# Kernel tuning notes

Hardware: AMD Instinct MI355X
Metric: run time of the kernel (lower is better)

Reference implementation:

```python
import jax, jax.numpy as jnp
import numpy as np

B, R = 2, 4096
N_COARSE, N_IMP = 48, 48
RAY_START, RAY_END = 0.1, 1.0
BOX_WARP = 2.0
C_PLANE, H_PLANE = 32, 256
HIDDEN = 64

_P = np.array([[[1, 0, 0], [0, 1, 0], [0, 0, 1]],
               [[1, 0, 0], [0, 0, 1], [0, 1, 0]],
               [[0, 0, 1], [1, 0, 0], [0, 1, 0]]], np.float32)
INV_PLANES = jnp.asarray(np.linalg.inv(_P))  # [3,3,3]


def _gs_one(f, g):
    # f: [C,H,W]; g: [M,2] in [-1,1]; bilinear, zeros padding, align_corners=False
    C, H, W = f.shape
    x = (g[:, 0] + 1.0) * (W / 2) - 0.5
    y = (g[:, 1] + 1.0) * (H / 2) - 0.5
    x0 = jnp.floor(x); y0 = jnp.floor(y)
    xi0 = x0.astype(jnp.int32); yi0 = y0.astype(jnp.int32)
    fx = x - x0; fy = y - y0
    out = jnp.zeros((C, g.shape[0]), f.dtype)
    for dx in (0, 1):
        for dy in (0, 1):
            xi = xi0 + dx; yi = yi0 + dy
            w = (fx if dx else 1.0 - fx) * (fy if dy else 1.0 - fy)
            valid = (xi >= 0) & (xi < W) & (yi >= 0) & (yi < H)
            val = f[:, jnp.clip(yi, 0, H - 1), jnp.clip(xi, 0, W - 1)]  # [C,M]
            out = out + jnp.where(valid, w, 0.0)[None, :] * val
    return out

grid_sample_2d = jax.vmap(_gs_one)


def sample_from_planes(plane_feats, coords):
    # plane_feats [B,3,C,H,W], coords [B,M,3] -> [B,M,C] (mean over planes)
    b, nP, C, H, W = plane_feats.shape
    c = (2.0 / BOX_WARP) * coords
    proj = jnp.einsum('bmk,pkj->bpmj', c, INV_PLANES)[..., :2]  # [B,3,M,2]
    out = grid_sample_2d(plane_feats.reshape(b * nP, C, H, W), proj.reshape(b * nP, -1, 2))
    return out.reshape(b, nP, C, -1).mean(1).transpose(0, 2, 1)


def decoder(tex_f, shp_f, W1, b1, W2, b2):
    x = jnp.concatenate([tex_f, shp_f], -1)          # [B,M,2C]
    h = jax.nn.softplus(x @ W1 + b1)
    o = h @ W2 + b2
    sigma = o[..., :1]
    rgb = jax.nn.sigmoid(o[..., 1:]) * (1 + 2 * 0.001) - 0.001
    return rgb, sigma


def ray_march(colors, densities, depths):
    # MipRayMarcher2: midpoint compositing, softplus(density-1), alpha compositing
    deltas = depths[:, :, 1:] - depths[:, :, :-1]
    c_mid = (colors[:, :, :-1] + colors[:, :, 1:]) * 0.5
    d_mid = (densities[:, :, :-1] + densities[:, :, 1:]) * 0.5
    z_mid = (depths[:, :, :-1] + depths[:, :, 1:]) * 0.5
    dens = jax.nn.softplus(d_mid - 1.0)
    alpha = 1.0 - jnp.exp(-dens * deltas)
    shifted = jnp.concatenate([jnp.ones_like(alpha[:, :, :1]), 1.0 - alpha + 1e-10], 2)
    weights = alpha * jnp.cumprod(shifted, 2)[:, :, :-1]
    rgb = (weights * c_mid).sum(2)
    wt = weights.sum(2)
    depth = jnp.nan_to_num((weights * z_mid).sum(2) / wt, posinf=0.0)
    depth = jnp.clip(depth, depths.min(), depths.max())
    return rgb * 2.0 - 1.0, depth, weights


def sample_pdf(bins, weights, u):
    # bins [P,Nb], weights [P,Nw], u [P,Ni] -> inverse-CDF samples [P,Ni]
    pdf = weights / jnp.sum(weights, -1, keepdims=True)
    cdf = jnp.cumsum(pdf, -1)
    cdf = jnp.concatenate([jnp.zeros_like(cdf[:, :1]), cdf], -1)
    inds = jax.vmap(lambda c, uu: jnp.searchsorted(c, uu, side='right'))(cdf, u)
    below = jnp.maximum(inds - 1, 0)
    above = jnp.minimum(inds, weights.shape[-1])
    cdf0 = jnp.take_along_axis(cdf, below, 1)
    cdf1 = jnp.take_along_axis(cdf, above, 1)
    b0 = jnp.take_along_axis(bins, below, 1)
    b1v = jnp.take_along_axis(bins, above, 1)
    denom = cdf1 - cdf0
    denom = jnp.where(denom < 1e-5, 1.0, denom)
    t = (u - cdf0) / denom
    return b0 + t * (b1v - b0)


def sample_importance(depths, weights, u):
    b, r, n1, _ = weights.shape  # n1 = N_COARSE - 1
    w = weights.reshape(b * r, n1)
    # max_pool1d(k=2, s=1, pad=1) then avg_pool1d(k=2, s=1), then +0.01 (weights >= 0)
    wp = jnp.concatenate([jnp.zeros_like(w[:, :1]), w, jnp.zeros_like(w[:, :1])], 1)
    w = jnp.maximum(wp[:, :-1], wp[:, 1:])
    w = 0.5 * (w[:, :-1] + w[:, 1:]) + 0.01
    z = depths.reshape(b * r, -1)
    z_mid = 0.5 * (z[:, :-1] + z[:, 1:])
    fine = sample_pdf(z_mid, w[:, 1:-1], u.reshape(b * r, -1))
    return jax.lax.stop_gradient(fine.reshape(b, r, -1, 1))  # .detach() in torch


def run_model(planes_tex, planes_shp, coords, W1, b1, W2, b2):
    tex_f = sample_from_planes(planes_tex, coords)
    shp_f = sample_from_planes(planes_shp, coords)
    return decoder(tex_f, shp_f, W1, b1, W2, b2)


def reference(planes_tex, planes_shp, ray_origins, ray_directions, W1, b1, W2, b2, strat_noise, imp_u):
    dirs = ray_directions / jnp.linalg.norm(ray_directions, axis=-1, keepdims=True)
    b, r, _ = ray_origins.shape
    delta = (RAY_END - RAY_START) / (N_COARSE - 1)
    base = RAY_START + delta * jnp.arange(N_COARSE, dtype=jnp.float32)
    depths_c = base.reshape(1, 1, N_COARSE, 1) + strat_noise * delta  # [B,R,Nc,1]
    coords_c = (ray_origins[:, :, None] + depths_c * dirs[:, :, None]).reshape(b, -1, 3)
    rgb_c, sig_c = run_model(planes_tex, planes_shp, coords_c, W1, b1, W2, b2)
    rgb_c = rgb_c.reshape(b, r, N_COARSE, 3)
    sig_c = sig_c.reshape(b, r, N_COARSE, 1)
    _, _, weights = ray_march(rgb_c, sig_c, depths_c)
    depths_f = sample_importance(depths_c, weights, imp_u)  # [B,R,Ni,1]
    coords_f = (ray_origins[:, :, None] + depths_f * dirs[:, :, None]).reshape(b, -1, 3)
    rgb_f, sig_f = run_model(planes_tex, planes_shp, coords_f, W1, b1, W2, b2)
    rgb_f = rgb_f.reshape(b, r, N_IMP, 3)
    sig_f = sig_f.reshape(b, r, N_IMP, 1)
    all_d = jnp.concatenate([depths_c, depths_f], 2)
    all_c = jnp.concatenate([rgb_c, rgb_f], 2)
    all_s = jnp.concatenate([sig_c, sig_f], 2)
    idx = jnp.argsort(all_d, axis=2)
    all_d = jnp.take_along_axis(all_d, idx, 2)
    all_c = jnp.take_along_axis(all_c, jnp.broadcast_to(idx, all_c.shape), 2)
    all_s = jnp.take_along_axis(all_s, idx, 2)
    rgb_final, depth_final, w_all = ray_march(all_c, all_s, all_d)
    return rgb_final, depth_final, w_all.sum(2)


def setup_inputs() -> dict:
    key = jax.random.key(0)
    ks = jax.random.split(key, 8)
    return {
        'planes_tex': jax.random.normal(ks[0], (B, 3, C_PLANE, H_PLANE, H_PLANE), jnp.float32),
        'planes_shp': jax.random.normal(ks[1], (B, 3, C_PLANE, H_PLANE, H_PLANE), jnp.float32),
        'ray_origins': 0.3 * jax.random.normal(ks[2], (B, R, 3), jnp.float32),
        'ray_directions': jax.random.normal(ks[3], (B, R, 3), jnp.float32),
        'W1': jax.random.normal(ks[4], (2 * C_PLANE, HIDDEN), jnp.float32) / np.sqrt(2 * C_PLANE),
        'b1': jnp.zeros((HIDDEN,), jnp.float32),
        'W2': jax.random.normal(ks[5], (HIDDEN, 4), jnp.float32) / np.sqrt(HIDDEN),
        'b2': jnp.zeros((4,), jnp.float32),
        'strat_noise': jax.random.uniform(ks[6], (B, R, N_COARSE, 1), jnp.float32),
        'imp_u': jax.random.uniform(ks[7], (B, R, N_IMP), jnp.float32),
    }
```

## Files before the change

kernel.cpp:

```cpp
#include <hip/hip_runtime.h>
#include <hip/hip_fp16.h>
#include <math.h>

#define NRAY 8192
#define NC_  48
#define NI_  48
#define HPL  256
#define HID  64
#define NPTS (NRAY * NC_)

typedef __attribute__((ext_vector_type(8))) short short8;
typedef __attribute__((ext_vector_type(4))) float f32x4;

__device__ __forceinline__ float softplusf(float x) {
    return fmaxf(x, 0.0f) + __logf(1.0f + __expf(-fabsf(x)));
}
__device__ __forceinline__ float sigmoidf(float x) {
    return 1.0f / (1.0f + __expf(-x));
}
__device__ __forceinline__ unsigned short f2bf(float f) {
    unsigned u = __float_as_uint(f);
    u += 0x7fffu + ((u >> 16) & 1u);
    return (unsigned short)(u >> 16);
}

#define TR_BLOCKS 3072
__global__ __launch_bounds__(256) void setup_kernel(
    const float* __restrict__ tex, const float* __restrict__ shp,
    __half* __restrict__ planes_cl,
    const float* __restrict__ W1, const float* __restrict__ b1, const float* __restrict__ W2,
    unsigned short* __restrict__ w1f, float* __restrict__ w2f, float* __restrict__ b1f,
    float* __restrict__ part_mn, float* __restrict__ part_mx,
    const float* __restrict__ noise)
{
    __shared__ __half t2[256][34];
    __shared__ float smn[4], smx[4];
    int b = blockIdx.x;
    int tid = threadIdx.x;
    if (b < TR_BLOCKS) {
        int p = b >> 8;
        int y = b & 255;
        const float* in = (p < 6) ? tex : shp;
        int pp    = (p < 6) ? p : p - 6;
        int choff = (p < 6) ? 0 : 32;
        const float* row = in + ((size_t)(pp * 32) * 256 + y) * 256;
#pragma unroll
        for (int c = 0; c < 32; ++c)
            t2[tid][c] = __float2half(row[(size_t)c * 65536 + tid]);
        __syncthreads();
        __half* outRow = planes_cl + ((size_t)(pp * 256 + y) * 256) * 64 + choff;
#pragma unroll
        for (int it = 0; it < 4; ++it) {
            int idx = it * 256 + tid;
            int x = idx >> 2, c8 = (idx & 3) * 8;
            *(uint4*)(outRow + (size_t)x * 64 + c8) = *(const uint4*)&t2[x][c8];
        }
    } else if (b == TR_BLOCKS) {
        int l = tid;
        if (l < 64) {
            int g = l >> 4, c = l & 15;
#pragma unroll
            for (int t = 0; t < 4; ++t) {
#pragma unroll
                for (int kb = 0; kb < 2; ++kb)
#pragma unroll
                    for (int j = 0; j < 8; ++j)
                        w1f[((t * 2 + kb) * 64 + l) * 8 + j] =
                            f2bf(W1[(kb * 32 + g * 8 + j) * HID + t * 16 + c]);
#pragma unroll
                for (int o = 0; o < 4; ++o) w2f[(t * 64 + l) * 4 + o] = W2[(t * 16 + c) * 4 + o];
                b1f[t * 64 + l] = b1[t * 16 + c];
            }
        }
    } else {
        int bl = b - TR_BLOCKS - 1;
        int gtid = bl * 256 + tid;
        float mn = INFINITY, mx = -INFINITY;
        for (int r = gtid; r < NRAY; r += 4096) {
            mn = fminf(mn, noise[r * NC_]);
            mx = fmaxf(mx, noise[r * NC_ + NC_ - 1]);
        }
#pragma unroll
        for (int mask = 1; mask <= 32; mask <<= 1) {
            mn = fminf(mn, __shfl_xor(mn, mask, 64));
            mx = fmaxf(mx, __shfl_xor(mx, mask, 64));
        }
        int wv = tid >> 6;
        if ((tid & 63) == 0) { smn[wv] = mn; smx[wv] = mx; }
        __syncthreads();
        if (tid == 0) {
#pragma unroll
            for (int i = 1; i < 4; ++i) { mn = fminf(mn, smn[i]); mx = fmaxf(mx, smx[i]); }
            const float delta = (1.0f - 0.1f) / (NC_ - 1);
            part_mn[bl] = 0.1f + mn * delta;
            part_mx[bl] = 0.1f + delta * 47.0f + mx * delta;
        }
    }
}

template<bool FINE>
__global__ __launch_bounds__(256, 8) void fused_sample_mlp(
    const __half* __restrict__ planes,
    const float* __restrict__ origins, const float* __restrict__ dirs,
    const float* __restrict__ noise,
    const float* __restrict__ impu,
    const float* __restrict__ depths_c,
    const float4* __restrict__ rgbs_c_in,
    float* __restrict__ depths_out,
    const unsigned short* __restrict__ w1f, const float* __restrict__ w2f,
    const float* __restrict__ b1f, const float* __restrict__ b2,
    float4* __restrict__ outRGBS)
{
    __shared__ unsigned short lds_x[32][72];
    __shared__ int s_tap[32][12][2];
    __shared__ float s_cdf[2][48];
    __shared__ float s_zm[2][48];

    int tid = threadIdx.x;
    int r0 = (blockIdx.x * 32) / NC_;

    if constexpr (FINE) {
        int wv = tid >> 6, lane = tid & 63;
        int r1 = (blockIdx.x * 32 + 31) / NC_;
        if (wv <= r1 - r0) {
            int ray = r0 + wv;
            float d = 0.f, sg = 0.f;
            if (lane < NC_) {
                d  = depths_c[ray * NC_ + lane];
                sg = rgbs_c_in[ray * NC_ + lane].w;
            }
            float dn = __shfl_down(d, 1, 64);
            float sn = __shfl_down(sg, 1, 64);
            bool iv = (lane < NC_ - 1);
            float zm = 0.5f * (d + dn);
            float alpha = 0.f, f = 1.0f;
            if (iv) {
                float dens = softplusf(0.5f * (sg + sn) - 1.0f);
                alpha = 1.0f - __expf(-dens * (dn - d));
                f = 1.0f - alpha + 1e-10f;
            }
            float x = f;
#pragma unroll
            for (int s = 1; s < 64; s <<= 1) {
                float t = __shfl_up(x, s, 64);
                if (lane >= s) x *= t;
            }
            float excl = __shfl_up(x, 1, 64);
            if (lane == 0) excl = 1.0f;
            float w = alpha * excl;
            float wprev = __shfl_up(w, 1, 64);
            float wmax;
            if (lane == 0) wmax = w;
            else if (lane == NC_ - 1) wmax = wprev;
            else wmax = fmaxf(wprev, w);
            float wmaxn = __shfl_down(wmax, 1, 64);
            float wb = 0.5f * (wmax + wmaxn) + 0.01f;
            float v = (lane >= 1 && lane <= 45) ? wb : 0.0f;
            float ssum = v;
#pragma unroll
            for (int mask = 1; mask <= 32; mask <<= 1) ssum += __shfl_xor(ssum, mask, 64);
            float pdf = v / ssum;
            float cum = pdf;
#pragma unroll
            for (int st = 1; st < 64; st <<= 1) {
                float t = __shfl_up(cum, st, 64);
                if (lane >= st) cum += t;
            }
            if (lane <= 45) s_cdf[wv][lane] = (lane == 0) ? 0.0f : cum;
            if (iv) s_zm[wv][lane] = zm;
        }
        __syncthreads();
    }

    if (tid < 96) {
        int p  = tid & 31;
        int pp = tid >> 5;
        int point = blockIdx.x * 32 + p;
        int ray = point / NC_;
        int bIdx = ray >> 12;

        float t;
        if constexpr (!FINE) {
            int s = point - ray * NC_;
            const float delta = (1.0f - 0.1f) / (NC_ - 1);
            t = 0.1f + delta * (float)s + noise[point] * delta;
        } else {
            int ridx = ray - r0;
            float u = impu[point];
            const float* cdf = s_cdf[ridx];
            const float* zmp = s_zm[ridx];
            int lo = 0, hi = 46;
            while (lo < hi) { int mid = (lo + hi) >> 1; if (cdf[mid] > u) hi = mid; else lo = mid + 1; }
            int below = max(lo - 1, 0);
            int above = min(lo, 45);
            float c0 = cdf[below], c1 = cdf[above];
            float b0 = zmp[below], b1v = zmp[above];
            float den = c1 - c0; if (den < 1e-5f) den = 1.0f;
            t = b0 + (u - c0) / den * (b1v - b0);
        }
        if (pp == 0) depths_out[point] = t;

        float ox = origins[ray * 3 + 0], oy = origins[ray * 3 + 1], oz = origins[ray * 3 + 2];
        float dx = dirs[ray * 3 + 0], dy = dirs[ray * 3 + 1], dz = dirs[ray * 3 + 2];
        float invn = 1.0f / sqrtf(dx * dx + dy * dy + dz * dz);
        dx *= invn; dy *= invn; dz *= invn;
        float px = ox + t * dx, py = oy + t * dy, pz = oz + t * dz;

        float U = (pp == 2) ? pz : px;
        float V = (pp == 0) ? py : ((pp == 1) ? pz : px);
        const float inv3 = 1.0f / 3.0f;

        float gx = (U + 1.0f) * 128.0f - 0.5f;
        float gy = (V + 1.0f) * 128.0f - 0.5f;
        float fgx = floorf(gx), fgy = floorf(gy);
        int x0 = (int)fgx, y0 = (int)fgy;
        float fx = gx - fgx, fy = gy - fgy;
#pragma unroll
        for (int k = 0; k < 4; ++k) {
            int dxk = k & 1, dyk = k >> 1;
            int xi = x0 + dxk, yi = y0 + dyk;
            float w = (dxk ? fx : 1.0f - fx) * (dyk ? fy : 1.0f - fy);
            bool valid = (xi >= 0) && (xi < HPL) && (yi >= 0) && (yi < HPL);
            int xc = min(max(xi, 0), HPL - 1);
            int yc = min(max(yi, 0), HPL - 1);
            int p3 = bIdx * 3 + pp;
            s_tap[p][pp * 4 + k][0] = (((p3 * HPL) + yc) * HPL + xc) * 64;
            s_tap[p][pp * 4 + k][1] = __float_as_int(valid ? w * inv3 : 0.0f);
        }
    }
    __syncthreads();

    {
        int p = tid >> 3, sub = tid & 7;
        int   off[12];
        float wv[12];
#pragma unroll
        for (int kk = 0; kk < 12; ++kk) {
            off[kk] = s_tap[p][kk][0];
            wv[kk]  = __int_as_float(s_tap[p][kk][1]);
        }
        __half2 acc2[4];
#pragma unroll
        for (int i = 0; i < 4; ++i) acc2[i] = __half2half2(__float2half(0.0f));
#pragma unroll
        for (int kk = 0; kk < 12; ++kk) {
            __half2 w2 = __half2half2(__float2half(wv[kk]));
            float4 v = *(const float4*)(planes + off[kk] + sub * 8);
            union { float4 f; __half2 h[4]; } u;
            u.f = v;
#pragma unroll
            for (int i = 0; i < 4; ++i) acc2[i] = __hfma2(u.h[i], w2, acc2[i]);
        }
        unsigned short u16[8];
#pragma unroll
        for (int i = 0; i < 4; ++i) {
            float2 f2 = __half22float2(acc2[i]);
            u16[2 * i]     = f2bf(f2.x);
            u16[2 * i + 1] = f2bf(f2.y);
        }
        *(uint4*)&lds_x[p][sub * 8] = *(uint4*)(u16);
    }
    __syncthreads();

    int lane = tid & 63, wave = tid >> 6;
    if (wave < 2) {
        int g = lane >> 4, c = lane & 15;
        int mrow = wave * 16 + c;
        short8 a0 = *(const short8*)(&lds_x[mrow][g * 8]);
        short8 a1 = *(const short8*)(&lds_x[mrow][32 + g * 8]);

        float o[4][4];
#pragma unroll
        for (int r = 0; r < 4; ++r)
#pragma unroll
            for (int q = 0; q < 4; ++q) o[r][q] = 0.0f;

#pragma unroll
        for (int t = 0; t < 4; ++t) {
            short8 bf0 = *(const short8*)(w1f + ((size_t)((t * 2 + 0) * 64 + lane)) * 8);
            short8 bf1 = *(const short8*)(w1f + ((size_t)((t * 2 + 1) * 64 + lane)) * 8);
            f32x4 z = {0.f, 0.f, 0.f, 0.f};
            z = __builtin_amdgcn_mfma_f32_16x16x32_bf16(a0, bf0, z, 0, 0, 0);
            z = __builtin_amdgcn_mfma_f32_16x16x32_bf16(a1, bf1, z, 0, 0, 0);
            float  b1s = b1f[t * 64 + lane];
            float4 w2  = *(const float4*)(w2f + (size_t)(t * 64 + lane) * 4);
#pragma unroll
            for (int r = 0; r < 4; ++r) {
                float sp = softplusf(z[r] + b1s);
                o[r][0] = fmaf(sp, w2.x, o[r][0]);
                o[r][1] = fmaf(sp, w2.y, o[r][1]);
                o[r][2] = fmaf(sp, w2.z, o[r][2]);
                o[r][3] = fmaf(sp, w2.w, o[r][3]);
            }
        }
#pragma unroll
        for (int mask = 1; mask <= 8; mask <<= 1)
#pragma unroll
            for (int r = 0; r < 4; ++r)
#pragma unroll
                for (int q = 0; q < 4; ++q) o[r][q] += __shfl_xor(o[r][q], mask, 64);

        if (c == 0) {
#pragma unroll
            for (int r = 0; r < 4; ++r) {
                int pt = blockIdx.x * 32 + wave * 16 + g * 4 + r;
                float sig = o[r][0] + b2[0];
                float rr = sigmoidf(o[r][1] + b2[1]) * 1.002f - 0.001f;
                float gg = sigmoidf(o[r][2] + b2[2]) * 1.002f - 0.001f;
                float bb = sigmoidf(o[r][3] + b2[3]) * 1.002f - 0.001f;
                outRGBS[pt] = make_float4(rr, gg, bb, sig);
            }
        }
    }
}

#define FM_WAVES 4
__global__ __launch_bounds__(256) void final_march(
    const float* __restrict__ depths_c, const float4* __restrict__ rgbs_c,
    const float* __restrict__ depths_f, const float4* __restrict__ rgbs_f,
    const float* __restrict__ part_mn, const float* __restrict__ part_mx,
    float* __restrict__ out)
{
    __shared__ float s_dc[FM_WAVES][NC_];
    __shared__ float s_df[FM_WAVES][NI_];
    __shared__ float s_md[FM_WAVES][96];
    __shared__ float s_ms[FM_WAVES][96];
    __shared__ float s_mr[FM_WAVES][96];
    __shared__ float s_mg[FM_WAVES][96];
    __shared__ float s_mb[FM_WAVES][96];

    int wave = threadIdx.x >> 6, lane = threadIdx.x & 63;
    int ray = blockIdx.x * FM_WAVES + wave;
    float* dcp = s_dc[wave];
    float* dfp = s_df[wave];
    float* mdp = s_md[wave];
    float* msp = s_ms[wave];
    float* mrp = s_mr[wave];
    float* mgp = s_mg[wave];
    float* mbp = s_mb[wave];

    float dcv = 0.f, dfv = 0.f;
    float4 c4 = make_float4(0, 0, 0, 0), f4 = make_float4(0, 0, 0, 0);
    if (lane < NC_) {
        dcv = depths_c[ray * NC_ + lane];
        dfv = depths_f[ray * NI_ + lane];
        dcp[lane] = dcv;
        dfp[lane] = dfv;
        c4 = rgbs_c[ray * NC_ + lane];
        f4 = rgbs_f[ray * NI_ + lane];
    }
    __syncthreads();

    if (lane < NC_) {
        int cntC = 0, rankF = 0, cntCle = 0;
#pragma unroll
        for (int j = 0; j < NC_; ++j) {
            float dfj = dfp[j];
            float dcj = dcp[j];
            cntC   += (dfj < dcv) ? 1 : 0;
            rankF  += ((dfj < dfv) || (dfj == dfv && j < lane)) ? 1 : 0;
            cntCle += (dcj <= dfv) ? 1 : 0;
        }
        int posC = lane + cntC;
        int posF = rankF + cntCle;
        mdp[posC] = dcv; msp[posC] = c4.w; mrp[posC] = c4.x; mgp[posC] = c4.y; mbp[posC] = c4.z;
        mdp[posF] = dfv; msp[posF] = f4.w; mrp[posF] = f4.x; mgp[posF] = f4.y; mbp[posF] = f4.z;
    }
    __syncthreads();

    int k0 = 2 * lane;
    int i0 = min(k0, 95), i1 = min(k0 + 1, 95), i2 = min(k0 + 2, 95);
    float d0 = mdp[i0], d1 = mdp[i1], d2 = mdp[i2];
    float sg0 = msp[i0], sg1 = msp[i1], sg2 = msp[i2];
    float r0 = mrp[i0], r1 = mrp[i1], r2 = mrp[i2];
    float g0 = mgp[i0], g1 = mgp[i1], g2 = mgp[i2];
    float bb0 = mbp[i0], bb1 = mbp[i1], bb2 = mbp[i2];

    bool v0 = (k0 < 95), v1 = (k0 + 1 < 95);
    float a0 = 0.f, a1 = 0.f, f0 = 1.f, f1 = 1.f;
    if (v0) {
        float dens = softplusf(0.5f * (sg0 + sg1) - 1.0f);
        a0 = 1.0f - __expf(-dens * (d1 - d0));
        f0 = 1.0f - a0 + 1e-10f;
    }
    if (v1) {
        float dens = softplusf(0.5f * (sg1 + sg2) - 1.0f);
        a1 = 1.0f - __expf(-dens * (d2 - d1));
        f1 = 1.0f - a1 + 1e-10f;
    }

    float pl = f0 * f1;
    float x = pl;
#pragma unroll
    for (int d = 1; d < 64; d <<= 1) {
        float t = __shfl_up(x, d, 64);
        if (lane >= d) x *= t;
    }
    float excl = __shfl_up(x, 1, 64);
    if (lane == 0) excl = 1.0f;
    float w0 = a0 * excl;
    float w1 = a1 * excl * f0;

    float accR = w0 * 0.5f * (r0 + r1) + w1 * 0.5f * (r1 + r2);
    float accG = w0 * 0.5f * (g0 + g1) + w1 * 0.5f * (g1 + g2);
    float accB = w0 * 0.5f * (bb0 + bb1) + w1 * 0.5f * (bb1 + bb2);
    float accD = w0 * 0.5f * (d0 + d1) + w1 * 0.5f * (d1 + d2);
    float accW = w0 + w1;
#pragma unroll
    for (int mask = 1; mask <= 32; mask <<= 1) {
        accR += __shfl_xor(accR, mask, 64);
        accG += __shfl_xor(accG, mask, 64);
        accB += __shfl_xor(accB, mask, 64);
        accD += __shfl_xor(accD, mask, 64);
        accW += __shfl_xor(accW, mask, 64);
    }

    float pmn = (lane < 16) ? part_mn[lane] : INFINITY;
    float pmx = (lane < 16) ? part_mx[lane] : -INFINITY;
#pragma unroll
    for (int mask = 1; mask <= 32; mask <<= 1) {
        pmn = fminf(pmn, __shfl_xor(pmn, mask, 64));
        pmx = fmaxf(pmx, __shfl_xor(pmx, mask, 64));
    }

    if (lane == 0) {
        float q = accD / accW;
        if (!isfinite(q)) q = 0.0f;
        q = fminf(fmaxf(q, pmn), pmx);
        out[ray * 3 + 0] = accR * 2.0f - 1.0f;
        out[ray * 3 + 1] = accG * 2.0f - 1.0f;
        out[ray * 3 + 2] = accB * 2.0f - 1.0f;
        out[3 * NRAY + ray] = q;
        out[4 * NRAY + ray] = accW;
    }
}

extern "C" void kernel_launch(void* const* d_in, const int* in_sizes, int n_in,
                              void* d_out, int out_size, void* d_ws, size_t ws_size,
                              hipStream_t stream)
{
    const float* planes_tex = (const float*)d_in[0];
    const float* planes_shp = (const float*)d_in[1];
    const float* origins    = (const float*)d_in[2];
    const float* raydirs    = (const float*)d_in[3];
    const float* W1 = (const float*)d_in[4];
    const float* b1 = (const float*)d_in[5];
    const float* W2 = (const float*)d_in[6];
    const float* b2 = (const float*)d_in[7];
    const float* noise = (const float*)d_in[8];
    const float* impu  = (const float*)d_in[9];
    float* out = (float*)d_out;

    char* ws = (char*)d_ws;
    __half*         planes_cl = (__half*)ws;
    unsigned short* w1f       = (unsigned short*)(ws + 50331648);
    float*          w2f       = (float*)(ws + 50339840);
    float*          b1f       = (float*)(ws + 50343936);
    float*          part_mn   = (float*)(ws + 50344960);
    float*          part_mx   = (float*)(ws + 50345024);
    float*  depths_c = (float*)(ws + 50345216);
    float*  depths_f = (float*)(ws + 51918080);
    float4* rgbs_c   = (float4*)(ws + 53490944);
    float4* rgbs_f   = (float4*)(ws + 59782400);

    setup_kernel<<<dim3(TR_BLOCKS + 1 + 16), dim3(256), 0, stream>>>(
        planes_tex, planes_shp, planes_cl, W1, b1, W2, w1f, w2f, b1f, part_mn, part_mx, noise);

    fused_sample_mlp<false><<<dim3(NPTS / 32), dim3(256), 0, stream>>>(
        planes_cl, origins, raydirs, noise, nullptr, nullptr, nullptr,
        depths_c, w1f, w2f, b1f, b2, rgbs_c);

    fused_sample_mlp<true><<<dim3(NPTS / 32), dim3(256), 0, stream>>>(
        planes_cl, origins, raydirs, nullptr, impu, depths_c, rgbs_c,
        depths_f, w1f, w2f, b1f, b2, rgbs_f);

    final_march<<<dim3(NRAY / FM_WAVES), dim3(256), 0, stream>>>(
        depths_c, rgbs_c, depths_f, rgbs_f, part_mn, part_mx, out);
}
```

Baseline: 282.3 us.

## Switch MLP to fp16 MFMA, vectorize plane transpose, precompute normalized ray directions

The first MLP layer now uses fp16 MFMA instead of bf16, so the fp16 accumulated features go straight to LDS without a per-element bf16 conversion. Tap weights are stored as packed half2, which removes a conversion in the gather loop. The plane transpose in setup now reads float4 vectors instead of scalars, and extra setup blocks precompute the normalized ray origin and direction per ray, so sample threads skip the sqrt and normalization. This adds a small workspace buffer, and the fp16 inputs to the MFMA have a narrower range than bf16.

```diff
diff --git a/kernel.cpp b/kernel.cpp
--- a/kernel.cpp
+++ b/kernel.cpp
@@ -9,7 +9,7 @@
 #define HID  64
 #define NPTS (NRAY * NC_)
 
-typedef __attribute__((ext_vector_type(8))) short short8;
+typedef __attribute__((ext_vector_type(8))) _Float16 half8;
 typedef __attribute__((ext_vector_type(4))) float f32x4;
 
 __device__ __forceinline__ float softplusf(float x) {
@@ -17,11 +17,6 @@
 }
 __device__ __forceinline__ float sigmoidf(float x) {
     return 1.0f / (1.0f + __expf(-x));
-}
-__device__ __forceinline__ unsigned short f2bf(float f) {
-    unsigned u = __float_as_uint(f);
-    u += 0x7fffu + ((u >> 16) & 1u);
-    return (unsigned short)(u >> 16);
 }
 
 #define TR_BLOCKS 3072
@@ -29,9 +24,11 @@
     const float* __restrict__ tex, const float* __restrict__ shp,
     __half* __restrict__ planes_cl,
     const float* __restrict__ W1, const float* __restrict__ b1, const float* __restrict__ W2,
-    unsigned short* __restrict__ w1f, float* __restrict__ w2f, float* __restrict__ b1f,
+    __half* __restrict__ w1f, float* __restrict__ w2f, float* __restrict__ b1f,
     float* __restrict__ part_mn, float* __restrict__ part_mx,
-    const float* __restrict__ noise)
+    const float* __restrict__ noise,
+    const float* __restrict__ origins, const float* __restrict__ dirs,
+    float* __restrict__ rayod)
 {
     __shared__ __half t2[256][34];
     __shared__ float smn[4], smx[4];
@@ -43,10 +40,18 @@
         const float* in = (p < 6) ? tex : shp;
         int pp    = (p < 6) ? p : p - 6;
         int choff = (p < 6) ? 0 : 32;
-        const float* row = in + ((size_t)(pp * 32) * 256 + y) * 256;
-#pragma unroll
-        for (int c = 0; c < 32; ++c)
-            t2[tid][c] = __float2half(row[(size_t)c * 65536 + tid]);
+        const float* base = in + ((size_t)(pp * 32) * 256 + y) * 256;
+        int lane6 = tid & 63;
+        int cb    = (tid >> 6) * 8;
+        int x0    = lane6 * 4;
+#pragma unroll
+        for (int i = 0; i < 8; ++i) {
+            float4 v = *(const float4*)(base + (size_t)(cb + i) * 65536 + x0);
+            t2[x0 + 0][cb + i] = __float2half(v.x);
+            t2[x0 + 1][cb + i] = __float2half(v.y);
+            t2[x0 + 2][cb + i] = __float2half(v.z);
+            t2[x0 + 3][cb + i] = __float2half(v.w);
+        }
         __syncthreads();
         __half* outRow = planes_cl + ((size_t)(pp * 256 + y) * 256) * 64 + choff;
 #pragma unroll
@@ -66,13 +71,13 @@
 #pragma unroll
                     for (int j = 0; j < 8; ++j)
                         w1f[((t * 2 + kb) * 64 + l) * 8 + j] =
-                            f2bf(W1[(kb * 32 + g * 8 + j) * HID + t * 16 + c]);
+                            __float2half(W1[(kb * 32 + g * 8 + j) * HID + t * 16 + c]);
 #pragma unroll
                 for (int o = 0; o < 4; ++o) w2f[(t * 64 + l) * 4 + o] = W2[(t * 16 + c) * 4 + o];
                 b1f[t * 64 + l] = b1[t * 16 + c];
             }
         }
-    } else {
+    } else if (b < TR_BLOCKS + 17) {
         int bl = b - TR_BLOCKS - 1;
         int gtid = bl * 256 + tid;
         float mn = INFINITY, mx = -INFINITY;
@@ -95,23 +100,33 @@
             part_mn[bl] = 0.1f + mn * delta;
             part_mx[bl] = 0.1f + delta * 47.0f + mx * delta;
         }
+    } else {
+        int ray = (b - TR_BLOCKS - 17) * 256 + tid;
+        float ox = origins[ray * 3 + 0], oy = origins[ray * 3 + 1], oz = origins[ray * 3 + 2];
+        float dx = dirs[ray * 3 + 0], dy = dirs[ray * 3 + 1], dz = dirs[ray * 3 + 2];
+        float invn = 1.0f / sqrtf(dx * dx + dy * dy + dz * dz);
+        dx *= invn; dy *= invn; dz *= invn;
+        float4 A4 = make_float4(ox, oy, oz, dx);
+        float4 B4 = make_float4(dy, dz, 0.0f, 0.0f);
+        *(float4*)(rayod + (size_t)ray * 8)     = A4;
+        *(float4*)(rayod + (size_t)ray * 8 + 4) = B4;
     }
 }
 
 template<bool FINE>
 __global__ __launch_bounds__(256, 8) void fused_sample_mlp(
     const __half* __restrict__ planes,
-    const float* __restrict__ origins, const float* __restrict__ dirs,
+    const float* __restrict__ rayod,
     const float* __restrict__ noise,
     const float* __restrict__ impu,
     const float* __restrict__ depths_c,
     const float4* __restrict__ rgbs_c_in,
     float* __restrict__ depths_out,
-    const unsigned short* __restrict__ w1f, const float* __restrict__ w2f,
+    const __half* __restrict__ w1f, const float* __restrict__ w2f,
     const float* __restrict__ b1f, const float* __restrict__ b2,
     float4* __restrict__ outRGBS)
 {
-    __shared__ unsigned short lds_x[32][72];
+    __shared__ __half lds_x[32][72];
     __shared__ int s_tap[32][12][2];
     __shared__ float s_cdf[2][48];
     __shared__ float s_zm[2][48];
@@ -200,11 +215,11 @@
         }
         if (pp == 0) depths_out[point] = t;
 
-        float ox = origins[ray * 3 + 0], oy = origins[ray * 3 + 1], oz = origins[ray * 3 + 2];
-        float dx = dirs[ray * 3 + 0], dy = dirs[ray * 3 + 1], dz = dirs[ray * 3 + 2];
-        float invn = 1.0f / sqrtf(dx * dx + dy * dy + dz * dz);
-        dx *= invn; dy *= invn; dz *= invn;
-        float px = ox + t * dx, py = oy + t * dy, pz = oz + t * dz;
+        const float4 A4 = *(const float4*)(rayod + (size_t)ray * 8);
+        const float4 B4 = *(const float4*)(rayod + (size_t)ray * 8 + 4);
+        float px = A4.x + t * A4.w;
+        float py = A4.y + t * B4.x;
+        float pz = A4.z + t * B4.y;
 
         float U = (pp == 2) ? pz : px;
         float V = (pp == 0) ? py : ((pp == 1) ? pz : px);
@@ -224,41 +239,35 @@
             int xc = min(max(xi, 0), HPL - 1);
             int yc = min(max(yi, 0), HPL - 1);
             int p3 = bIdx * 3 + pp;
+            __half2 hw2 = __half2half2(__float2half(valid ? w * inv3 : 0.0f));
             s_tap[p][pp * 4 + k][0] = (((p3 * HPL) + yc) * HPL + xc) * 64;
-            s_tap[p][pp * 4 + k][1] = __float_as_int(valid ? w * inv3 : 0.0f);
+            s_tap[p][pp * 4 + k][1] = *(const int*)&hw2;
         }
     }
     __syncthreads();
 
     {
         int p = tid >> 3, sub = tid & 7;
-        int   off[12];
-        float wv[12];
+        int off[12];
+        int wb[12];
 #pragma unroll
         for (int kk = 0; kk < 12; ++kk) {
             off[kk] = s_tap[p][kk][0];
-            wv[kk]  = __int_as_float(s_tap[p][kk][1]);
+            wb[kk]  = s_tap[p][kk][1];
         }
         __half2 acc2[4];
 #pragma unroll
         for (int i = 0; i < 4; ++i) acc2[i] = __half2half2(__float2half(0.0f));
 #pragma unroll
         for (int kk = 0; kk < 12; ++kk) {
-            __half2 w2 = __half2half2(__float2half(wv[kk]));
+            __half2 w2 = *(const __half2*)&wb[kk];
             float4 v = *(const float4*)(planes + off[kk] + sub * 8);
             union { float4 f; __half2 h[4]; } u;
             u.f = v;
 #pragma unroll
             for (int i = 0; i < 4; ++i) acc2[i] = __hfma2(u.h[i], w2, acc2[i]);
         }
-        unsigned short u16[8];
-#pragma unroll
-        for (int i = 0; i < 4; ++i) {
-            float2 f2 = __half22float2(acc2[i]);
-            u16[2 * i]     = f2bf(f2.x);
-            u16[2 * i + 1] = f2bf(f2.y);
-        }
-        *(uint4*)&lds_x[p][sub * 8] = *(uint4*)(u16);
+        *(uint4*)&lds_x[p][sub * 8] = *(const uint4*)&acc2[0];
     }
     __syncthreads();
 
@@ -266,8 +275,8 @@
     if (wave < 2) {
         int g = lane >> 4, c = lane & 15;
         int mrow = wave * 16 + c;
-        short8 a0 = *(const short8*)(&lds_x[mrow][g * 8]);
-        short8 a1 = *(const short8*)(&lds_x[mrow][32 + g * 8]);
+        half8 a0 = *(const half8*)(&lds_x[mrow][g * 8]);
+        half8 a1 = *(const half8*)(&lds_x[mrow][32 + g * 8]);
 
         float o[4][4];
 #pragma unroll
@@ -277,11 +286,11 @@
 
 #pragma unroll
         for (int t = 0; t < 4; ++t) {
-            short8 bf0 = *(const short8*)(w1f + ((size_t)((t * 2 + 0) * 64 + lane)) * 8);
-            short8 bf1 = *(const short8*)(w1f + ((size_t)((t * 2 + 1) * 64 + lane)) * 8);
+            half8 bf0 = *(const half8*)(w1f + ((size_t)((t * 2 + 0) * 64 + lane)) * 8);
+            half8 bf1 = *(const half8*)(w1f + ((size_t)((t * 2 + 1) * 64 + lane)) * 8);
             f32x4 z = {0.f, 0.f, 0.f, 0.f};
-            z = __builtin_amdgcn_mfma_f32_16x16x32_bf16(a0, bf0, z, 0, 0, 0);
-            z = __builtin_amdgcn_mfma_f32_16x16x32_bf16(a1, bf1, z, 0, 0, 0);
+            z = __builtin_amdgcn_mfma_f32_16x16x32_f16(a0, bf0, z, 0, 0, 0);
+            z = __builtin_amdgcn_mfma_f32_16x16x32_f16(a1, bf1, z, 0, 0, 0);
             float  b1s = b1f[t * 64 + lane];
             float4 w2  = *(const float4*)(w2f + (size_t)(t * 64 + lane) * 4);
 #pragma unroll
@@ -453,7 +462,7 @@
 
     char* ws = (char*)d_ws;
     __half*         planes_cl = (__half*)ws;
-    unsigned short* w1f       = (unsigned short*)(ws + 50331648);
+    __half*         w1f       = (__half*)(ws + 50331648);
     float*          w2f       = (float*)(ws + 50339840);
     float*          b1f       = (float*)(ws + 50343936);
     float*          part_mn   = (float*)(ws + 50344960);
@@ -462,16 +471,18 @@
     float*  depths_f = (float*)(ws + 51918080);
     float4* rgbs_c   = (float4*)(ws + 53490944);
     float4* rgbs_f   = (float4*)(ws + 59782400);
-
-    setup_kernel<<<dim3(TR_BLOCKS + 1 + 16), dim3(256), 0, stream>>>(
-        planes_tex, planes_shp, planes_cl, W1, b1, W2, w1f, w2f, b1f, part_mn, part_mx, noise);
+    float*  rayod    = (float*)(ws + 66073856);
+
+    setup_kernel<<<dim3(TR_BLOCKS + 1 + 16 + 32), dim3(256), 0, stream>>>(
+        planes_tex, planes_shp, planes_cl, W1, b1, W2, w1f, w2f, b1f, part_mn, part_mx,
+        noise, origins, raydirs, rayod);
 
     fused_sample_mlp<false><<<dim3(NPTS / 32), dim3(256), 0, stream>>>(
-        planes_cl, origins, raydirs, noise, nullptr, nullptr, nullptr,
+        planes_cl, rayod, noise, nullptr, nullptr, nullptr,
         depths_c, w1f, w2f, b1f, b2, rgbs_c);
 
     fused_sample_mlp<true><<<dim3(NPTS / 32), dim3(256), 0, stream>>>(
-        planes_cl, origins, raydirs, nullptr, impu, depths_c, rgbs_c,
+        planes_cl, rayod, nullptr, impu, depths_c, rgbs_c,
         depths_f, w1f, w2f, b1f, b2, rgbs_f);
 
     final_march<<<dim3(NRAY / FM_WAVES), dim3(256), 0, stream>>>(
```

After: 280.4 us. No clear change (-0.7%).
